# Optimization experiments

Hardware: AMD Instinct MI355X
Metric: run time of the kernel (lower is better)

## Reference

```python
import jax, jax.numpy as jnp
import numpy as np

S = 2   # scale_factor
K = 5   # k_up
M = 48  # m_channels
KE = 3  # k_encoder


def conv2d(x, w, b, pad):
    # NCHW conv, stride 1, symmetric padding (matches nn.Conv2d(padding=pad))
    y = jax.lax.conv_general_dilated(
        x, w, window_strides=(1, 1), padding=[(pad, pad), (pad, pad)],
        dimension_numbers=("NCHW", "OIHW", "NCHW"))
    return y + b[None, :, None, None]


def setup_inputs() -> dict:
    key = jax.random.key(0)
    k1, k2, k3, k4, k5 = jax.random.split(key, 5)
    C_in = 64
    x = jax.random.normal(k1, (8, C_in, 128, 128), dtype=jnp.float32)
    w_compress = jax.random.normal(k2, (M, C_in, 1, 1), dtype=jnp.float32) * 0.1
    b_compress = jax.random.normal(k3, (M,), dtype=jnp.float32) * 0.05
    w_encoder = jax.random.normal(k4, ((K * S) ** 2, M, KE, KE), dtype=jnp.float32) * 0.05
    b_encoder = jax.random.normal(k5, ((K * S) ** 2,), dtype=jnp.float32) * 0.05
    return {"x": x, "w_compress": w_compress, "b_compress": b_compress,
            "w_encoder": w_encoder, "b_encoder": b_encoder}


def reference(x, w_compress, b_compress, w_encoder, b_encoder):
    B, C, H, W = x.shape
    # mask branch: compress -> relu -> encoder -> softmax over k_up^2
    y = jax.nn.relu(conv2d(x, w_compress, b_compress, pad=0))
    y = conv2d(y, w_encoder, b_encoder, pad=KE // 2)          # [B, (K*S)^2, H, W]
    y = y.reshape(B, S * S, K * K, H, W)
    y = jax.nn.softmax(y, axis=2)
    # unfold x with kernel K, pad K//2, stride 1 -> [B, C, K*K, H, W]
    p = K // 2
    xpad = jnp.pad(x, ((0, 0), (0, 0), (p, p), (p, p)))
    unf = jnp.stack([xpad[:, :, i:i + H, j:j + W]
                     for i in range(K) for j in range(K)], axis=2)
    # per-subpixel softmax-weighted patch sum; channel layout (scale_idx, C)
    out = jnp.einsum("bskhw,bckhw->bschw", y, unf)            # [B, S^2, C, H, W]
    out = out.reshape(B, S * S * C, H, W)
    # PixelShuffle(S): view (B, C_out, r, r, H, W) -> (B, C_out, H, r, W, r)
    r = S
    c_out = (S * S * C) // (r * r)
    out = out.reshape(B, c_out, r, r, H, W).transpose(0, 1, 4, 2, 5, 3)
    return out.reshape(B, c_out, H * r, W * r)
```

## Files before the change

kernel.cpp:

```cpp
#include <hip/hip_runtime.h>

#define HW 16384

typedef __bf16 bf16x8 __attribute__((ext_vector_type(8)));
typedef __bf16 bf16x4 __attribute__((ext_vector_type(4)));
typedef float  f32x4  __attribute__((ext_vector_type(4)));
typedef float  f32x2  __attribute__((ext_vector_type(2)));

__global__ __launch_bounds__(256)
void prep_xt(const float* __restrict__ x, __bf16* __restrict__ xt) {
    __shared__ float lds[256 * 65];
    const int b = blockIdx.x & 7, chunk = blockIdx.x >> 3;
    const int t = threadIdx.x;
    const int pos0 = chunk * 256;
    const float* xb = x + (size_t)b * 64 * HW + pos0;
    for (int c = 0; c < 64; ++c)
        lds[t * 65 + c] = xb[(size_t)c * HW + t];
    __syncthreads();
    __bf16* o = xt + ((size_t)b * HW + pos0 + t) * 64;
    #pragma unroll
    for (int j = 0; j < 8; ++j) {
        bf16x8 v;
        #pragma unroll
        for (int e = 0; e < 8; ++e) v[e] = (__bf16)lds[t * 65 + j * 8 + e];
        *(bf16x8*)(o + j * 8) = v;
    }
}

__global__ __launch_bounds__(256)
void prep_w(const float* __restrict__ we, const float* __restrict__ wc,
            __bf16* __restrict__ wt, __bf16* __restrict__ wcb) {
    int idx = blockIdx.x * 256 + threadIdx.x;
    if (idx < 112 * 448) {
        int e = idx / 448, k = idx % 448;
        float v = 0.f;
        if (e < 100 && k < 432) {
            int t = k / 48, m = k % 48;
            v = we[(e * 48 + m) * 9 + t];
        }
        wt[idx] = (__bf16)v;
    } else {
        idx -= 112 * 448;
        if (idx < 48 * 64) wcb[idx] = (__bf16)wc[idx];
    }
}

__global__ __launch_bounds__(256, 2)
void carafe_weights(const __bf16* __restrict__ xt,
                    const __bf16* __restrict__ wcb, const float* __restrict__ bc,
                    const __bf16* __restrict__ wt, const float* __restrict__ be,
                    _Float16* __restrict__ wn) {
    __shared__ __align__(16) char smem[59392];
    __bf16*    y1  = (__bf16*)smem;
    _Float16*  lgt = (_Float16*)smem;

    const int tid = threadIdx.x;
    const int lane = tid & 63, wv = tid >> 6;
    const int lgp = lane >> 4, lr = lane & 15;
    const int b = blockIdx.x & 7, tile = blockIdx.x >> 3;
    const int h0 = (tile >> 3) << 4, w0 = (tile & 7) << 4;

    bf16x8 bw[3][2];
    float bias1[3];
    #pragma unroll
    for (int nt = 0; nt < 3; ++nt) {
        bias1[nt] = bc[nt * 16 + lr];
        #pragma unroll
        for (int kc = 0; kc < 2; ++kc)
            bw[nt][kc] = *(const bf16x8*)(wcb + (nt * 16 + lr) * 64 + kc * 32 + lgp * 8);
    }
    for (int pt = wv; pt < 21; pt += 4) {
        int pos = pt * 16 + lr;
        int pr = (pos * 1821) >> 15;  int pc = pos - pr * 18;
        int hy = h0 - 1 + pr, wx = w0 - 1 + pc;
        bool ok = (hy >= 0) & (hy < 128) & (wx >= 0) & (wx < 128);
        const __bf16* ap = xt + ((size_t)b * HW + (ok ? (hy * 128 + wx) : 0)) * 64 + lgp * 8;
        bf16x8 a0 = *(const bf16x8*)ap;
        bf16x8 a1 = *(const bf16x8*)(ap + 32);
        if (!ok) {
            #pragma unroll
            for (int e = 0; e < 8; ++e) { a0[e] = (__bf16)0.f; a1[e] = (__bf16)0.f; }
        }
        #pragma unroll
        for (int nt = 0; nt < 3; ++nt) {
            f32x4 cc = {bias1[nt], bias1[nt], bias1[nt], bias1[nt]};
            cc = __builtin_amdgcn_mfma_f32_16x16x32_bf16(a0, bw[nt][0], cc, 0, 0, 0);
            cc = __builtin_amdgcn_mfma_f32_16x16x32_bf16(a1, bw[nt][1], cc, 0, 0, 0);
            #pragma unroll
            for (int r = 0; r < 4; ++r) {
                int posw = pt * 16 + lgp * 4 + r;
                int pr2 = (posw * 1821) >> 15;  int pc2 = posw - pr2 * 18;
                int hy2 = h0 - 1 + pr2, wx2 = w0 - 1 + pc2;
                bool ok2 = (hy2 >= 0) & (hy2 < 128) & (wx2 >= 0) & (wx2 < 128);
                float v = ok2 ? fmaxf(cc[r], 0.f) : 0.f;
                y1[posw * 56 + nt * 16 + lr] = (__bf16)v;
            }
        }
    }
    for (int i = tid; i < 448; i += 256)
        y1[336 * 56 + i] = (__bf16)0.f;
    __syncthreads();

    f32x4 acc[4][7];
    #pragma unroll
    for (int ot = 0; ot < 7; ++ot) {
        int o_ = ot * 16 + lr;
        float bz = (o_ < 100) ? be[o_] : 0.f;
        #pragma unroll
        for (int i = 0; i < 4; ++i) acc[i][ot] = {bz, bz, bz, bz};
    }
    const int ptg0 = wv * 4;

    auto ldA = [&](bf16x8 A[4], int kc) {
        int Kb = kc * 32 + lgp * 8;
        int t  = (Kb * 683) >> 15;  int m0 = Kb - t * 48;
        int ty = (t * 11) >> 5;     int tx = t - ty * 3;
        int base = ty * 18 + lr + tx;
        #pragma unroll
        for (int i = 0; i < 4; ++i)
            A[i] = *(const bf16x8*)(y1 + ((ptg0 + i) * 18 + base) * 56 + m0);
    };
    auto ldB = [&](bf16x8 B[7], int kc) {
        #pragma unroll
        for (int j = 0; j < 7; ++j)
            B[j] = *(const bf16x8*)(wt + (j * 16 + lr) * 448 + kc * 32 + lgp * 8);
    };
    auto mm = [&](bf16x8 A[4], bf16x8 B[7]) {
        #pragma unroll
        for (int i = 0; i < 4; ++i)
            #pragma unroll
            for (int j = 0; j < 7; ++j)
                acc[i][j] = __builtin_amdgcn_mfma_f32_16x16x32_bf16(A[i], B[j], acc[i][j], 0, 0, 0);
    };

    bf16x8 A0[4], B0[7], A1[4], B1[7];
    ldA(A0, 0); ldB(B0, 0);
    #pragma unroll
    for (int kc = 0; kc < 14; kc += 2) {
        if (kc + 1 < 14) { ldA(A1, kc + 1); ldB(B1, kc + 1); }
        mm(A0, B0);
        if (kc + 2 < 14) { ldA(A0, kc + 2); ldB(B0, kc + 2); }
        if (kc + 1 < 14) mm(A1, B1);
    }
    __syncthreads();

    #pragma unroll
    for (int i = 0; i < 4; ++i)
        #pragma unroll
        for (int j = 0; j < 7; ++j) {
            int o_ = j * 16 + lr;
            #pragma unroll
            for (int r = 0; r < 4; ++r) {
                int p = (ptg0 + i) * 16 + lgp * 4 + r;
                lgt[p * 116 + o_] = (_Float16)acc[i][j][r];
            }
        }
    __syncthreads();

    const int p = tid;
    float wt_[100];
    const _Float16* lrow = lgt + p * 116;
    #pragma unroll
    for (int g = 0; g < 4; ++g) {
        float v[25];
        #pragma unroll
        for (int k = 0; k < 25; ++k) v[k] = (float)lrow[g * 25 + k];
        float mx = v[0];
        #pragma unroll
        for (int k = 1; k < 25; ++k) mx = fmaxf(mx, v[k]);
        float s = 0.f;
        #pragma unroll
        for (int k = 0; k < 25; ++k) { v[k] = __expf(v[k] - mx); s += v[k]; }
        float inv = 1.f / s;
        #pragma unroll
        for (int k = 0; k < 25; ++k) wt_[g * 25 + k] = v[k] * inv;
    }
    _Float16* wp = wn + (size_t)b * 100 * HW + tile * 256 + p;
    #pragma unroll
    for (int j = 0; j < 100; ++j) wp[(size_t)j * HW] = (_Float16)wt_[j];
}

__global__ __launch_bounds__(512, 4)
void carafe_apply(const __bf16* __restrict__ xt, const _Float16* __restrict__ wn,
                  float* __restrict__ out) {
    __shared__ __bf16 lx[400 * 68];

    const int tid = threadIdx.x;
    const int b = blockIdx.x & 7, tile = blockIdx.x >> 3;
    const int h0 = (tile >> 3) << 4, w0 = (tile & 7) << 4;

    const int l8 = tid & 7, pg = tid >> 3;
    for (int it = 0; it < 7; ++it) {
        int pos = it * 64 + pg;
        if (pos < 400) {
            int r = pos / 20, q = pos % 20;
            int hy = h0 - 2 + r, wx = w0 - 2 + q;
            bf16x8 v = {};
            if (hy >= 0 && hy < 128 && wx >= 0 && wx < 128)
                v = *(const bf16x8*)(xt + ((size_t)b * HW + hy * 128 + wx) * 64 + l8 * 8);
            bf16x4 vlo = {v[0], v[1], v[2], v[3]};
            bf16x4 vhi = {v[4], v[5], v[6], v[7]};
            *(bf16x4*)(lx + pos * 68 + l8 * 8)     = vlo;
            *(bf16x4*)(lx + pos * 68 + l8 * 8 + 4) = vhi;
        }
    }

    const int pix = tid & 255, sgrp = tid >> 8;
    const int py = pix >> 4, px = pix & 15;
    const int h = h0 + py, w = w0 + px;
    float wt_[50];
    const _Float16* wp = wn + ((size_t)b * 100 + sgrp * 50) * HW + tile * 256 + pix;
    #pragma unroll
    for (int j = 0; j < 50; ++j) wt_[j] = (float)wp[(size_t)j * HW];

    __syncthreads();

    float* ob = out + (size_t)b * 256 * HW;
    #pragma unroll 1
    for (int cq = 0; cq < 16; ++cq) {
        f32x2 a0 = {0.f, 0.f}, a1 = {0.f, 0.f}, a2 = {0.f, 0.f}, a3 = {0.f, 0.f};
        #pragma unroll
        for (int ki = 0; ki < 5; ++ki) {
            const int rowbase = (py + ki) * 20 + px;
            #pragma unroll
            for (int kj = 0; kj < 5; ++kj) {
                uint2 u = *(const uint2*)(lx + (rowbase + kj) * 68 + cq * 4);
                f32x2 xlo = { __uint_as_float(u.x << 16), __uint_as_float(u.x & 0xffff0000u) };
                f32x2 xhi = { __uint_as_float(u.y << 16), __uint_as_float(u.y & 0xffff0000u) };
                float wA = wt_[ki * 5 + kj];
                float wB = wt_[25 + ki * 5 + kj];
                a0 += xlo * wA;
                a1 += xhi * wA;
                a2 += xlo * wB;
                a3 += xhi * wB;
            }
        }
        size_t base0 = ((size_t)(sgrp * 32 + cq) * 256 + 2 * h) * 256 + 2 * w;
        *(f32x2*)(ob + base0)       = a0;
        *(f32x2*)(ob + base0 + 256) = a1;
        size_t base1 = base0 + (size_t)16 * 256 * 256;
        *(f32x2*)(ob + base1)       = a2;
        *(f32x2*)(ob + base1 + 256) = a3;
    }
}

extern "C" void kernel_launch(void* const* d_in, const int* in_sizes, int n_in,
                              void* d_out, int out_size, void* d_ws, size_t ws_size,
                              hipStream_t stream) {
    const float* x  = (const float*)d_in[0];
    const float* wc = (const float*)d_in[1];
    const float* bc = (const float*)d_in[2];
    const float* we = (const float*)d_in[3];
    const float* be = (const float*)d_in[4];
    float* out = (float*)d_out;

    __bf16*   xt  = (__bf16*)d_ws;
    __bf16*   wte = (__bf16*)((char*)d_ws + 16777216);
    __bf16*   wcb = (__bf16*)((char*)d_ws + 16777216 + 100352);
    _Float16* wn  = (_Float16*)((char*)d_ws + 16883712);

    prep_xt<<<512, 256, 0, stream>>>(x, xt);
    prep_w<<<208, 256, 0, stream>>>(we, wc, wte, wcb);
    carafe_weights<<<512, 256, 0, stream>>>(xt, wcb, bc, wte, be, wn);
    carafe_apply<<<512, 512, 0, stream>>>(xt, wn, out);
}
```

Baseline: 95.39 us.

## Fuse mask-weight and apply kernels, merge prep kernels into one launch

```diff
diff --git a/kernel.cpp b/kernel.cpp
--- a/kernel.cpp
+++ b/kernel.cpp
@@ -8,51 +8,58 @@
 typedef float  f32x2  __attribute__((ext_vector_type(2)));
 
 __global__ __launch_bounds__(256)
-void prep_xt(const float* __restrict__ x, __bf16* __restrict__ xt) {
+void prep_all(const float* __restrict__ x, const float* __restrict__ we,
+              const float* __restrict__ wc,
+              __bf16* __restrict__ xt, __bf16* __restrict__ wt, __bf16* __restrict__ wcb) {
+    const int t = threadIdx.x;
+    if (blockIdx.x >= 512) {
+        int idx = (blockIdx.x - 512) * 256 + t;
+        if (idx < 112 * 448) {
+            int e = idx / 448, k = idx % 448;
+            float v = 0.f;
+            if (e < 100 && k < 432) {
+                int tt = k / 48, m = k % 48;
+                v = we[(e * 48 + m) * 9 + tt];
+            }
+            wt[idx] = (__bf16)v;
+        } else {
+            idx -= 112 * 448;
+            if (idx < 48 * 64) wcb[idx] = (__bf16)wc[idx];
+        }
+        return;
+    }
     __shared__ float lds[256 * 65];
     const int b = blockIdx.x & 7, chunk = blockIdx.x >> 3;
-    const int t = threadIdx.x;
     const int pos0 = chunk * 256;
     const float* xb = x + (size_t)b * 64 * HW + pos0;
     for (int c = 0; c < 64; ++c)
         lds[t * 65 + c] = xb[(size_t)c * HW + t];
     __syncthreads();
-    __bf16* o = xt + ((size_t)b * HW + pos0 + t) * 64;
-    #pragma unroll
-    for (int j = 0; j < 8; ++j) {
-        bf16x8 v;
-        #pragma unroll
-        for (int e = 0; e < 8; ++e) v[e] = (__bf16)lds[t * 65 + j * 8 + e];
-        *(bf16x8*)(o + j * 8) = v;
+    const int q = t & 3, pp = t >> 2;
+    #pragma unroll
+    for (int it = 0; it < 4; ++it) {
+        int pos = it * 64 + pp;
+        __bf16* o = xt + ((size_t)b * HW + pos0 + pos) * 64 + q * 16;
+        bf16x8 v0, v1;
+        #pragma unroll
+        for (int e = 0; e < 8; ++e) {
+            v0[e] = (__bf16)lds[pos * 65 + q * 16 + e];
+            v1[e] = (__bf16)lds[pos * 65 + q * 16 + 8 + e];
+        }
+        *(bf16x8*)o       = v0;
+        *(bf16x8*)(o + 8) = v1;
     }
 }
 
-__global__ __launch_bounds__(256)
-void prep_w(const float* __restrict__ we, const float* __restrict__ wc,
-            __bf16* __restrict__ wt, __bf16* __restrict__ wcb) {
-    int idx = blockIdx.x * 256 + threadIdx.x;
-    if (idx < 112 * 448) {
-        int e = idx / 448, k = idx % 448;
-        float v = 0.f;
-        if (e < 100 && k < 432) {
-            int t = k / 48, m = k % 48;
-            v = we[(e * 48 + m) * 9 + t];
-        }
-        wt[idx] = (__bf16)v;
-    } else {
-        idx -= 112 * 448;
-        if (idx < 48 * 64) wcb[idx] = (__bf16)wc[idx];
-    }
-}
-
-__global__ __launch_bounds__(256, 2)
-void carafe_weights(const __bf16* __restrict__ xt,
-                    const __bf16* __restrict__ wcb, const float* __restrict__ bc,
-                    const __bf16* __restrict__ wt, const float* __restrict__ be,
-                    _Float16* __restrict__ wn) {
+__global__ __launch_bounds__(512, 4)
+void carafe_fused(const __bf16* __restrict__ xt,
+                  const __bf16* __restrict__ wcb, const float* __restrict__ bc,
+                  const __bf16* __restrict__ wt, const float* __restrict__ be,
+                  float* __restrict__ out) {
     __shared__ __align__(16) char smem[59392];
     __bf16*    y1  = (__bf16*)smem;
     _Float16*  lgt = (_Float16*)smem;
+    __bf16*    lx  = (__bf16*)smem;
 
     const int tid = threadIdx.x;
     const int lane = tid & 63, wv = tid >> 6;
@@ -60,92 +67,82 @@
     const int b = blockIdx.x & 7, tile = blockIdx.x >> 3;
     const int h0 = (tile >> 3) << 4, w0 = (tile & 7) << 4;
 
-    bf16x8 bw[3][2];
-    float bias1[3];
-    #pragma unroll
-    for (int nt = 0; nt < 3; ++nt) {
-        bias1[nt] = bc[nt * 16 + lr];
-        #pragma unroll
-        for (int kc = 0; kc < 2; ++kc)
-            bw[nt][kc] = *(const bf16x8*)(wcb + (nt * 16 + lr) * 64 + kc * 32 + lgp * 8);
-    }
-    for (int pt = wv; pt < 21; pt += 4) {
-        int pos = pt * 16 + lr;
-        int pr = (pos * 1821) >> 15;  int pc = pos - pr * 18;
-        int hy = h0 - 1 + pr, wx = w0 - 1 + pc;
-        bool ok = (hy >= 0) & (hy < 128) & (wx >= 0) & (wx < 128);
-        const __bf16* ap = xt + ((size_t)b * HW + (ok ? (hy * 128 + wx) : 0)) * 64 + lgp * 8;
-        bf16x8 a0 = *(const bf16x8*)ap;
-        bf16x8 a1 = *(const bf16x8*)(ap + 32);
-        if (!ok) {
-            #pragma unroll
-            for (int e = 0; e < 8; ++e) { a0[e] = (__bf16)0.f; a1[e] = (__bf16)0.f; }
-        }
+    {
+        bf16x8 bw[3][2];
+        float bias1[3];
         #pragma unroll
         for (int nt = 0; nt < 3; ++nt) {
-            f32x4 cc = {bias1[nt], bias1[nt], bias1[nt], bias1[nt]};
-            cc = __builtin_amdgcn_mfma_f32_16x16x32_bf16(a0, bw[nt][0], cc, 0, 0, 0);
-            cc = __builtin_amdgcn_mfma_f32_16x16x32_bf16(a1, bw[nt][1], cc, 0, 0, 0);
-            #pragma unroll
-            for (int r = 0; r < 4; ++r) {
-                int posw = pt * 16 + lgp * 4 + r;
-                int pr2 = (posw * 1821) >> 15;  int pc2 = posw - pr2 * 18;
-                int hy2 = h0 - 1 + pr2, wx2 = w0 - 1 + pc2;
-                bool ok2 = (hy2 >= 0) & (hy2 < 128) & (wx2 >= 0) & (wx2 < 128);
-                float v = ok2 ? fmaxf(cc[r], 0.f) : 0.f;
-                y1[posw * 56 + nt * 16 + lr] = (__bf16)v;
-            }
-        }
-    }
-    for (int i = tid; i < 448; i += 256)
-        y1[336 * 56 + i] = (__bf16)0.f;
-    __syncthreads();
-
-    f32x4 acc[4][7];
+            bias1[nt] = bc[nt * 16 + lr];
+            #pragma unroll
+            for (int kc = 0; kc < 2; ++kc)
+                bw[nt][kc] = *(const bf16x8*)(wcb + (nt * 16 + lr) * 64 + kc * 32 + lgp * 8);
+        }
+        for (int pt = wv; pt < 21; pt += 8) {
+            int pos = pt * 16 + lr;
+            int pr = (pos * 1821) >> 15;  int pc = pos - pr * 18;
+            int hy = h0 - 1 + pr, wx = w0 - 1 + pc;
+            bool ok = (hy >= 0) & (hy < 128) & (wx >= 0) & (wx < 128);
+            const __bf16* ap = xt + ((size_t)b * HW + (ok ? (hy * 128 + wx) : 0)) * 64 + lgp * 8;
+            bf16x8 a0 = *(const bf16x8*)ap;
+            bf16x8 a1 = *(const bf16x8*)(ap + 32);
+            if (!ok) {
+                #pragma unroll
+                for (int e = 0; e < 8; ++e) { a0[e] = (__bf16)0.f; a1[e] = (__bf16)0.f; }
+            }
+            #pragma unroll
+            for (int nt = 0; nt < 3; ++nt) {
+                f32x4 cc = {bias1[nt], bias1[nt], bias1[nt], bias1[nt]};
+                cc = __builtin_amdgcn_mfma_f32_16x16x32_bf16(a0, bw[nt][0], cc, 0, 0, 0);
+                cc = __builtin_amdgcn_mfma_f32_16x16x32_bf16(a1, bw[nt][1], cc, 0, 0, 0);
+                #pragma unroll
+                for (int r = 0; r < 4; ++r) {
+                    int posw = pt * 16 + lgp * 4 + r;
+                    int pr2 = (posw * 1821) >> 15;  int pc2 = posw - pr2 * 18;
+                    int hy2 = h0 - 1 + pr2, wx2 = w0 - 1 + pc2;
+                    bool ok2 = (hy2 >= 0) & (hy2 < 128) & (wx2 >= 0) & (wx2 < 128);
+                    float v = ok2 ? fmaxf(cc[r], 0.f) : 0.f;
+                    y1[posw * 56 + nt * 16 + lr] = (__bf16)v;
+                }
+            }
+        }
+    }
+    if (tid < 448) y1[336 * 56 + tid] = (__bf16)0.f;
+    __syncthreads();
+
+    f32x4 acc[2][7];
+    const int ptg0 = wv * 2;
     #pragma unroll
     for (int ot = 0; ot < 7; ++ot) {
         int o_ = ot * 16 + lr;
         float bz = (o_ < 100) ? be[o_] : 0.f;
         #pragma unroll
-        for (int i = 0; i < 4; ++i) acc[i][ot] = {bz, bz, bz, bz};
-    }
-    const int ptg0 = wv * 4;
-
-    auto ldA = [&](bf16x8 A[4], int kc) {
-        int Kb = kc * 32 + lgp * 8;
-        int t  = (Kb * 683) >> 15;  int m0 = Kb - t * 48;
-        int ty = (t * 11) >> 5;     int tx = t - ty * 3;
-        int base = ty * 18 + lr + tx;
-        #pragma unroll
-        for (int i = 0; i < 4; ++i)
-            A[i] = *(const bf16x8*)(y1 + ((ptg0 + i) * 18 + base) * 56 + m0);
-    };
-    auto ldB = [&](bf16x8 B[7], int kc) {
-        #pragma unroll
-        for (int j = 0; j < 7; ++j)
-            B[j] = *(const bf16x8*)(wt + (j * 16 + lr) * 448 + kc * 32 + lgp * 8);
-    };
-    auto mm = [&](bf16x8 A[4], bf16x8 B[7]) {
-        #pragma unroll
-        for (int i = 0; i < 4; ++i)
+        for (int i = 0; i < 2; ++i) acc[i][ot] = {bz, bz, bz, bz};
+    }
+    {
+        #pragma unroll 2
+        for (int kc = 0; kc < 14; ++kc) {
+            int Kb = kc * 32 + lgp * 8;
+            int t  = (Kb * 683) >> 15;  int m0 = Kb - t * 48;
+            int ty = (t * 11) >> 5;     int tx = t - ty * 3;
+            int base = ty * 18 + lr + tx;
+            bf16x8 A[2], B[7];
+            #pragma unroll
+            for (int i = 0; i < 2; ++i)
+                A[i] = *(const bf16x8*)(y1 + ((ptg0 + i) * 18 + base) * 56 + m0);
             #pragma unroll
             for (int j = 0; j < 7; ++j)
-                acc[i][j] = __builtin_amdgcn_mfma_f32_16x16x32_bf16(A[i], B[j], acc[i][j], 0, 0, 0);
-    };
-
-    bf16x8 A0[4], B0[7], A1[4], B1[7];
-    ldA(A0, 0); ldB(B0, 0);
-    #pragma unroll
-    for (int kc = 0; kc < 14; kc += 2) {
-        if (kc + 1 < 14) { ldA(A1, kc + 1); ldB(B1, kc + 1); }
-        mm(A0, B0);
-        if (kc + 2 < 14) { ldA(A0, kc + 2); ldB(B0, kc + 2); }
-        if (kc + 1 < 14) mm(A1, B1);
-    }
-    __syncthreads();
-
-    #pragma unroll
-    for (int i = 0; i < 4; ++i)
+                B[j] = *(const bf16x8*)(wt + (j * 16 + lr) * 448 + kc * 32 + lgp * 8);
+            #pragma unroll
+            for (int i = 0; i < 2; ++i)
+                #pragma unroll
+                for (int j = 0; j < 7; ++j)
+                    acc[i][j] = __builtin_amdgcn_mfma_f32_16x16x32_bf16(A[i], B[j], acc[i][j], 0, 0, 0);
+        }
+    }
+    __syncthreads();
+
+    #pragma unroll
+    for (int i = 0; i < 2; ++i)
         #pragma unroll
         for (int j = 0; j < 7; ++j) {
             int o_ = j * 16 + lr;
@@ -157,62 +154,57 @@
         }
     __syncthreads();
 
-    const int p = tid;
-    float wt_[100];
-    const _Float16* lrow = lgt + p * 116;
-    #pragma unroll
-    for (int g = 0; g < 4; ++g) {
-        float v[25];
-        #pragma unroll
-        for (int k = 0; k < 25; ++k) v[k] = (float)lrow[g * 25 + k];
-        float mx = v[0];
-        #pragma unroll
-        for (int k = 1; k < 25; ++k) mx = fmaxf(mx, v[k]);
-        float s = 0.f;
-        #pragma unroll
-        for (int k = 0; k < 25; ++k) { v[k] = __expf(v[k] - mx); s += v[k]; }
-        float inv = 1.f / s;
-        #pragma unroll
-        for (int k = 0; k < 25; ++k) wt_[g * 25 + k] = v[k] * inv;
-    }
-    _Float16* wp = wn + (size_t)b * 100 * HW + tile * 256 + p;
-    #pragma unroll
-    for (int j = 0; j < 100; ++j) wp[(size_t)j * HW] = (_Float16)wt_[j];
-}
-
-__global__ __launch_bounds__(512, 4)
-void carafe_apply(const __bf16* __restrict__ xt, const _Float16* __restrict__ wn,
-                  float* __restrict__ out) {
-    __shared__ __bf16 lx[400 * 68];
-
-    const int tid = threadIdx.x;
-    const int b = blockIdx.x & 7, tile = blockIdx.x >> 3;
-    const int h0 = (tile >> 3) << 4, w0 = (tile & 7) << 4;
-
     const int l8 = tid & 7, pg = tid >> 3;
+    bf16x8 hv[7];
+    int     hpos[7];
+    #pragma unroll
     for (int it = 0; it < 7; ++it) {
         int pos = it * 64 + pg;
+        hpos[it] = pos;
+        bf16x8 v = {};
         if (pos < 400) {
-            int r = pos / 20, q = pos % 20;
-            int hy = h0 - 2 + r, wx = w0 - 2 + q;
-            bf16x8 v = {};
+            int r = pos / 20, qq = pos % 20;
+            int hy = h0 - 2 + r, wx = w0 - 2 + qq;
             if (hy >= 0 && hy < 128 && wx >= 0 && wx < 128)
                 v = *(const bf16x8*)(xt + ((size_t)b * HW + hy * 128 + wx) * 64 + l8 * 8);
-            bf16x4 vlo = {v[0], v[1], v[2], v[3]};
-            bf16x4 vhi = {v[4], v[5], v[6], v[7]};
-            *(bf16x4*)(lx + pos * 68 + l8 * 8)     = vlo;
-            *(bf16x4*)(lx + pos * 68 + l8 * 8 + 4) = vhi;
-        }
+        }
+        hv[it] = v;
     }
 
     const int pix = tid & 255, sgrp = tid >> 8;
     const int py = pix >> 4, px = pix & 15;
     const int h = h0 + py, w = w0 + px;
     float wt_[50];
-    const _Float16* wp = wn + ((size_t)b * 100 + sgrp * 50) * HW + tile * 256 + pix;
-    #pragma unroll
-    for (int j = 0; j < 50; ++j) wt_[j] = (float)wp[(size_t)j * HW];
-
+    {
+        const _Float16* lrow = lgt + pix * 116 + sgrp * 50;
+        #pragma unroll
+        for (int g = 0; g < 2; ++g) {
+            float v[25];
+            #pragma unroll
+            for (int k = 0; k < 25; ++k) v[k] = (float)lrow[g * 25 + k];
+            float mx = v[0];
+            #pragma unroll
+            for (int k = 1; k < 25; ++k) mx = fmaxf(mx, v[k]);
+            float s = 0.f;
+            #pragma unroll
+            for (int k = 0; k < 25; ++k) { v[k] = __expf(v[k] - mx); s += v[k]; }
+            float inv = 1.f / s;
+            #pragma unroll
+            for (int k = 0; k < 25; ++k) wt_[g * 25 + k] = v[k] * inv;
+        }
+    }
+    __syncthreads();
+
+    #pragma unroll
+    for (int it = 0; it < 7; ++it) {
+        int pos = hpos[it];
+        if (pos < 400) {
+            bf16x4 vlo = {hv[it][0], hv[it][1], hv[it][2], hv[it][3]};
+            bf16x4 vhi = {hv[it][4], hv[it][5], hv[it][6], hv[it][7]};
+            *(bf16x4*)(lx + pos * 68 + l8 * 8)     = vlo;
+            *(bf16x4*)(lx + pos * 68 + l8 * 8 + 4) = vhi;
+        }
+    }
     __syncthreads();
 
     float* ob = out + (size_t)b * 256 * HW;
@@ -254,13 +246,10 @@
     const float* be = (const float*)d_in[4];
     float* out = (float*)d_out;
 
-    __bf16*   xt  = (__bf16*)d_ws;
-    __bf16*   wte = (__bf16*)((char*)d_ws + 16777216);
-    __bf16*   wcb = (__bf16*)((char*)d_ws + 16777216 + 100352);
-    _Float16* wn  = (_Float16*)((char*)d_ws + 16883712);
-
-    prep_xt<<<512, 256, 0, stream>>>(x, xt);
-    prep_w<<<208, 256, 0, stream>>>(we, wc, wte, wcb);
-    carafe_weights<<<512, 256, 0, stream>>>(xt, wcb, bc, wte, be, wn);
-    carafe_apply<<<512, 512, 0, stream>>>(xt, wn, out);
+    __bf16* xt  = (__bf16*)d_ws;
+    __bf16* wte = (__bf16*)((char*)d_ws + 16777216);
+    __bf16* wcb = (__bf16*)((char*)d_ws + 16777216 + 100352);
+
+    prep_all<<<512 + 208, 256, 0, stream>>>(x, we, wc, xt, wte, wcb);
+    carafe_fused<<<512, 512, 0, stream>>>(xt, wcb, bc, wte, be, out);
 }
```

Measured after the change: 100.3 us. +5.2%, slower.

## Pack softmax weights in pairs, coalesce xt stores, batch halo loads before LDS writes

Applied to the files above, without the earlier changes.

```diff
diff --git a/kernel.cpp b/kernel.cpp
--- a/kernel.cpp
+++ b/kernel.cpp
@@ -17,13 +17,19 @@
     for (int c = 0; c < 64; ++c)
         lds[t * 65 + c] = xb[(size_t)c * HW + t];
     __syncthreads();
-    __bf16* o = xt + ((size_t)b * HW + pos0 + t) * 64;
-    #pragma unroll
-    for (int j = 0; j < 8; ++j) {
-        bf16x8 v;
-        #pragma unroll
-        for (int e = 0; e < 8; ++e) v[e] = (__bf16)lds[t * 65 + j * 8 + e];
-        *(bf16x8*)(o + j * 8) = v;
+    const int q = t & 3, pp = t >> 2;
+    #pragma unroll
+    for (int it = 0; it < 4; ++it) {
+        int pos = it * 64 + pp;
+        __bf16* o = xt + ((size_t)b * HW + pos0 + pos) * 64 + q * 16;
+        bf16x8 v0, v1;
+        #pragma unroll
+        for (int e = 0; e < 8; ++e) {
+            v0[e] = (__bf16)lds[pos * 65 + q * 16 + e];
+            v1[e] = (__bf16)lds[pos * 65 + q * 16 + 8 + e];
+        }
+        *(bf16x8*)o       = v0;
+        *(bf16x8*)(o + 8) = v1;
     }
 }
 
@@ -49,7 +55,7 @@
 void carafe_weights(const __bf16* __restrict__ xt,
                     const __bf16* __restrict__ wcb, const float* __restrict__ bc,
                     const __bf16* __restrict__ wt, const float* __restrict__ be,
-                    _Float16* __restrict__ wn) {
+                    unsigned int* __restrict__ wnp) {
     __shared__ __align__(16) char smem[59392];
     __bf16*    y1  = (__bf16*)smem;
     _Float16*  lgt = (_Float16*)smem;
@@ -60,40 +66,42 @@
     const int b = blockIdx.x & 7, tile = blockIdx.x >> 3;
     const int h0 = (tile >> 3) << 4, w0 = (tile & 7) << 4;
 
-    bf16x8 bw[3][2];
-    float bias1[3];
-    #pragma unroll
-    for (int nt = 0; nt < 3; ++nt) {
-        bias1[nt] = bc[nt * 16 + lr];
-        #pragma unroll
-        for (int kc = 0; kc < 2; ++kc)
-            bw[nt][kc] = *(const bf16x8*)(wcb + (nt * 16 + lr) * 64 + kc * 32 + lgp * 8);
-    }
-    for (int pt = wv; pt < 21; pt += 4) {
-        int pos = pt * 16 + lr;
-        int pr = (pos * 1821) >> 15;  int pc = pos - pr * 18;
-        int hy = h0 - 1 + pr, wx = w0 - 1 + pc;
-        bool ok = (hy >= 0) & (hy < 128) & (wx >= 0) & (wx < 128);
-        const __bf16* ap = xt + ((size_t)b * HW + (ok ? (hy * 128 + wx) : 0)) * 64 + lgp * 8;
-        bf16x8 a0 = *(const bf16x8*)ap;
-        bf16x8 a1 = *(const bf16x8*)(ap + 32);
-        if (!ok) {
-            #pragma unroll
-            for (int e = 0; e < 8; ++e) { a0[e] = (__bf16)0.f; a1[e] = (__bf16)0.f; }
-        }
+    {
+        bf16x8 bw[3][2];
+        float bias1[3];
         #pragma unroll
         for (int nt = 0; nt < 3; ++nt) {
-            f32x4 cc = {bias1[nt], bias1[nt], bias1[nt], bias1[nt]};
-            cc = __builtin_amdgcn_mfma_f32_16x16x32_bf16(a0, bw[nt][0], cc, 0, 0, 0);
-            cc = __builtin_amdgcn_mfma_f32_16x16x32_bf16(a1, bw[nt][1], cc, 0, 0, 0);
-            #pragma unroll
-            for (int r = 0; r < 4; ++r) {
-                int posw = pt * 16 + lgp * 4 + r;
-                int pr2 = (posw * 1821) >> 15;  int pc2 = posw - pr2 * 18;
-                int hy2 = h0 - 1 + pr2, wx2 = w0 - 1 + pc2;
-                bool ok2 = (hy2 >= 0) & (hy2 < 128) & (wx2 >= 0) & (wx2 < 128);
-                float v = ok2 ? fmaxf(cc[r], 0.f) : 0.f;
-                y1[posw * 56 + nt * 16 + lr] = (__bf16)v;
+            bias1[nt] = bc[nt * 16 + lr];
+            #pragma unroll
+            for (int kc = 0; kc < 2; ++kc)
+                bw[nt][kc] = *(const bf16x8*)(wcb + (nt * 16 + lr) * 64 + kc * 32 + lgp * 8);
+        }
+        for (int pt = wv; pt < 21; pt += 4) {
+            int pos = pt * 16 + lr;
+            int pr = (pos * 1821) >> 15;  int pc = pos - pr * 18;
+            int hy = h0 - 1 + pr, wx = w0 - 1 + pc;
+            bool ok = (hy >= 0) & (hy < 128) & (wx >= 0) & (wx < 128);
+            const __bf16* ap = xt + ((size_t)b * HW + (ok ? (hy * 128 + wx) : 0)) * 64 + lgp * 8;
+            bf16x8 a0 = *(const bf16x8*)ap;
+            bf16x8 a1 = *(const bf16x8*)(ap + 32);
+            if (!ok) {
+                #pragma unroll
+                for (int e = 0; e < 8; ++e) { a0[e] = (__bf16)0.f; a1[e] = (__bf16)0.f; }
+            }
+            #pragma unroll
+            for (int nt = 0; nt < 3; ++nt) {
+                f32x4 cc = {bias1[nt], bias1[nt], bias1[nt], bias1[nt]};
+                cc = __builtin_amdgcn_mfma_f32_16x16x32_bf16(a0, bw[nt][0], cc, 0, 0, 0);
+                cc = __builtin_amdgcn_mfma_f32_16x16x32_bf16(a1, bw[nt][1], cc, 0, 0, 0);
+                #pragma unroll
+                for (int r = 0; r < 4; ++r) {
+                    int posw = pt * 16 + lgp * 4 + r;
+                    int pr2 = (posw * 1821) >> 15;  int pc2 = posw - pr2 * 18;
+                    int hy2 = h0 - 1 + pr2, wx2 = w0 - 1 + pc2;
+                    bool ok2 = (hy2 >= 0) & (hy2 < 128) & (wx2 >= 0) & (wx2 < 128);
+                    float v = ok2 ? fmaxf(cc[r], 0.f) : 0.f;
+                    y1[posw * 56 + nt * 16 + lr] = (__bf16)v;
+                }
             }
         }
     }
@@ -175,13 +183,20 @@
         #pragma unroll
         for (int k = 0; k < 25; ++k) wt_[g * 25 + k] = v[k] * inv;
     }
-    _Float16* wp = wn + (size_t)b * 100 * HW + tile * 256 + p;
-    #pragma unroll
-    for (int j = 0; j < 100; ++j) wp[(size_t)j * HW] = (_Float16)wt_[j];
+    #pragma unroll
+    for (int s2 = 0; s2 < 2; ++s2) {
+        unsigned int* wp = wnp + (size_t)(b * 2 + s2) * 25 * HW + tile * 256 + p;
+        #pragma unroll
+        for (int k = 0; k < 25; ++k) {
+            unsigned short lo = __builtin_bit_cast(unsigned short, (_Float16)wt_[s2 * 50 + k]);
+            unsigned short hi = __builtin_bit_cast(unsigned short, (_Float16)wt_[s2 * 50 + 25 + k]);
+            wp[(size_t)k * HW] = (unsigned int)lo | ((unsigned int)hi << 16);
+        }
+    }
 }
 
 __global__ __launch_bounds__(512, 4)
-void carafe_apply(const __bf16* __restrict__ xt, const _Float16* __restrict__ wn,
+void carafe_apply(const __bf16* __restrict__ xt, const unsigned int* __restrict__ wnp,
                   float* __restrict__ out) {
     __shared__ __bf16 lx[400 * 68];
 
@@ -190,29 +205,44 @@
     const int h0 = (tile >> 3) << 4, w0 = (tile & 7) << 4;
 
     const int l8 = tid & 7, pg = tid >> 3;
+    bf16x8 hv[7];
+    #pragma unroll
     for (int it = 0; it < 7; ++it) {
         int pos = it * 64 + pg;
+        bf16x8 v = {};
         if (pos < 400) {
             int r = pos / 20, q = pos % 20;
             int hy = h0 - 2 + r, wx = w0 - 2 + q;
-            bf16x8 v = {};
             if (hy >= 0 && hy < 128 && wx >= 0 && wx < 128)
                 v = *(const bf16x8*)(xt + ((size_t)b * HW + hy * 128 + wx) * 64 + l8 * 8);
-            bf16x4 vlo = {v[0], v[1], v[2], v[3]};
-            bf16x4 vhi = {v[4], v[5], v[6], v[7]};
-            *(bf16x4*)(lx + pos * 68 + l8 * 8)     = vlo;
-            *(bf16x4*)(lx + pos * 68 + l8 * 8 + 4) = vhi;
-        }
+        }
+        hv[it] = v;
     }
 
     const int pix = tid & 255, sgrp = tid >> 8;
     const int py = pix >> 4, px = pix & 15;
     const int h = h0 + py, w = w0 + px;
     float wt_[50];
-    const _Float16* wp = wn + ((size_t)b * 100 + sgrp * 50) * HW + tile * 256 + pix;
-    #pragma unroll
-    for (int j = 0; j < 50; ++j) wt_[j] = (float)wp[(size_t)j * HW];
-
+    {
+        const unsigned int* wp = wnp + (size_t)(b * 2 + sgrp) * 25 * HW + tile * 256 + pix;
+        #pragma unroll
+        for (int k = 0; k < 25; ++k) {
+            unsigned int u = wp[(size_t)k * HW];
+            wt_[k]      = (float)__builtin_bit_cast(_Float16, (unsigned short)(u & 0xffffu));
+            wt_[25 + k] = (float)__builtin_bit_cast(_Float16, (unsigned short)(u >> 16));
+        }
+    }
+
+    #pragma unroll
+    for (int it = 0; it < 7; ++it) {
+        int pos = it * 64 + pg;
+        if (pos < 400) {
+            bf16x4 vlo = {hv[it][0], hv[it][1], hv[it][2], hv[it][3]};
+            bf16x4 vhi = {hv[it][4], hv[it][5], hv[it][6], hv[it][7]};
+            *(bf16x4*)(lx + pos * 68 + l8 * 8)     = vlo;
+            *(bf16x4*)(lx + pos * 68 + l8 * 8 + 4) = vhi;
+        }
+    }
     __syncthreads();
 
     float* ob = out + (size_t)b * 256 * HW;
@@ -254,13 +284,13 @@
     const float* be = (const float*)d_in[4];
     float* out = (float*)d_out;
 
-    __bf16*   xt  = (__bf16*)d_ws;
-    __bf16*   wte = (__bf16*)((char*)d_ws + 16777216);
-    __bf16*   wcb = (__bf16*)((char*)d_ws + 16777216 + 100352);
-    _Float16* wn  = (_Float16*)((char*)d_ws + 16883712);
+    __bf16*       xt  = (__bf16*)d_ws;
+    __bf16*       wte = (__bf16*)((char*)d_ws + 16777216);
+    __bf16*       wcb = (__bf16*)((char*)d_ws + 16777216 + 100352);
+    unsigned int* wnp = (unsigned int*)((char*)d_ws + 16883712);
 
     prep_xt<<<512, 256, 0, stream>>>(x, xt);
     prep_w<<<208, 256, 0, stream>>>(we, wc, wte, wcb);
-    carafe_weights<<<512, 256, 0, stream>>>(xt, wcb, bc, wte, be, wn);
-    carafe_apply<<<512, 512, 0, stream>>>(xt, wn, out);
-}
+    carafe_weights<<<512, 256, 0, stream>>>(xt, wcb, bc, wte, be, wnp);
+    carafe_apply<<<512, 512, 0, stream>>>(xt, wnp, out);
+}
```

Result: faster. 92.33 us (-3.2%).
